# Optimization experiments

Measured on AMD Instinct MI355X. Metric: run time of the kernel, lower is better.

## Reference

```python
import jax, jax.numpy as jnp
import numpy as np

FEATURES, NEURONS, THETA, TAU, H = 128, 512, 256, 1.0, 0.1
B, T = 64, 2048

def setup_inputs() -> dict:
    key = jax.random.key(0)
    ks = jax.random.split(key, 8)
    IN = FEATURES + NEURONS
    s = lambda n: 1.0 / np.sqrt(n)
    return {
        "I": jax.random.normal(ks[0], (B, T, FEATURES), dtype=jnp.float32),
        "W_ih": jax.random.uniform(ks[1], (THETA, IN), jnp.float32, -s(THETA), s(THETA)),
        "W_hh": jax.random.uniform(ks[2], (THETA, THETA), jnp.float32, -s(THETA), s(THETA)),
        "b_ih": jax.random.uniform(ks[3], (THETA,), jnp.float32, -s(THETA), s(THETA)),
        "b_hh": jax.random.uniform(ks[4], (THETA,), jnp.float32, -s(THETA), s(THETA)),
        "W_out": jax.random.uniform(ks[5], (NEURONS, THETA), jnp.float32, -s(THETA), s(THETA)),
        "b_out": jax.random.uniform(ks[6], (NEURONS,), jnp.float32, -s(THETA), s(THETA)),
        "A": jax.random.normal(ks[7], (NEURONS,), dtype=jnp.float32),
    }

def reference(I, W_ih, W_hh, b_ih, b_hh, W_out, b_out, A):
    batch = I.shape[0]
    x0 = jnp.zeros((batch, NEURONS), I.dtype)
    s0 = jnp.zeros((batch, THETA), I.dtype)

    def step(carry, I_t):
        x, s = carry
        cat = jnp.concatenate([x, I_t], axis=-1)            # [B, neurons+features]
        s_new = jnp.tanh(cat @ W_ih.T + b_ih + s @ W_hh.T + b_hh)  # single-step tanh RNN
        f = jax.nn.relu(s_new @ W_out.T + b_out)            # [B, neurons]
        # implicit-Euler ODE update
        x_next = (x + H * (f * A)) / (1.0 + H * (1.0 / TAU + f))
        return (x_next, s_new), x_next

    _, xs = jax.lax.scan(step, (x0, s0), jnp.swapaxes(I, 0, 1))  # [T, B, neurons]
    return jnp.swapaxes(xs, 0, 1)  # [B, T, neurons]
```

## Files before the change

kernel.cpp:

```cpp
#include <hip/hip_runtime.h>
#include <hip/hip_fp16.h>

#define TT 2048
typedef unsigned int uint32;
typedef unsigned long long uint64;
typedef unsigned short ushort;

typedef _Float16 half2v __attribute__((ext_vector_type(2)));

#if defined(__has_builtin)
#  if __has_builtin(__builtin_amdgcn_fdot2)
#    define HAVE_DOT2 1
#  endif
#endif
#ifndef HAVE_DOT2
#  define HAVE_DOT2 0
#endif

#define WREG_N (2 * 176 * 512)
#define EXA_N  (2 * 64 * 2 * 256)

__device__ __forceinline__ float dot2(uint32 a, uint32 w, float c)
{
#if HAVE_DOT2
    return __builtin_amdgcn_fdot2(__builtin_bit_cast(half2v, a),
                                  __builtin_bit_cast(half2v, w), c, false);
#else
    half2v av = __builtin_bit_cast(half2v, a);
    half2v wv = __builtin_bit_cast(half2v, w);
    c = fmaf((float)av.x, (float)wv.x, c);
    return fmaf((float)av.y, (float)wv.y, c);
#endif
}

__device__ __forceinline__ uint32 pkh(float a, float b)
{
    __half ha = __float2half(a), hb = __float2half(b);
    ushort ua = *reinterpret_cast<ushort*>(&ha);
    ushort ub = *reinterpret_cast<ushort*>(&hb);
    return (uint32)ua | ((uint32)ub << 16);
}

__device__ __forceinline__ float getSlice(const float* __restrict__ W_ih,
                                          const float* __restrict__ W_hh,
                                          int g, int j, int k)
{
    if (k < 256) return W_ih[j * 640 + 256 * g + k];
    if (k < 384) return W_hh[j * 256 + 128 * g + (k - 256)];
    return W_ih[j * 640 + 512 + 64 * g + (k - 384)];
}

__global__ void prep_kernel(const float* __restrict__ W_ih,
                            const float* __restrict__ W_hh,
                            const float* __restrict__ W_out,
                            uint32* __restrict__ WREGH,
                            uint64* __restrict__ exS)
{
    int idx = blockIdx.x * blockDim.x + threadIdx.x;
    if (idx < WREG_N) {
        int tid  = idx & 511;
        int q    = idx >> 9;
        int g    = q / 176;
        int slot = q % 176;
        float lo, hi;
        if (slot < 112) {
            int j = tid >> 1, h = tid & 1;
            int k0 = 2 * (112 * h + slot);
            lo = getSlice(W_ih, W_hh, g, j, k0);
            hi = getSlice(W_ih, W_hh, g, j, k0 + 1);
        } else {
            int s  = slot - 112;
            int ii = s >> 2, m = s & 3;
            int nloc = tid >> 1, hh = tid & 1;
            int n  = 256 * g + nloc;
            int k0 = 128 * hh + 8 * ii + 2 * m;
            lo = W_out[n * 256 + k0];
            hi = W_out[n * 256 + k0 + 1];
        }
        WREGH[idx] = pkh(lo, hi);
    } else if (idx < WREG_N + EXA_N) {
        exS[idx - WREG_N] = 0ULL;
    }
}

__device__ __forceinline__ void bar_lds()
{
    asm volatile("s_waitcnt lgkmcnt(0)" ::: "memory");
    __builtin_amdgcn_s_barrier();
    asm volatile("" ::: "memory");
}

__global__ __launch_bounds__(512, 2)
void scan_kernel(const float* __restrict__ I,
                 const float* __restrict__ b_ih, const float* __restrict__ b_hh,
                 const float* __restrict__ b_out, const float* __restrict__ A,
                 const uint32* __restrict__ WREGH,
                 uint64* exS,
                 float* __restrict__ out)
{
    __shared__ uint4 apk4[2][56];
    __shared__ uint4 s4pk[32];
    __shared__ float xf32[256];

    const int tid = threadIdx.x;
    const int bid = blockIdx.x;
    const int b   = bid & 63;
    const int g   = bid >> 6;

    uint32 wA[112], wB[64];
    const uint32* wsrc = WREGH + (size_t)g * (176 * 512) + tid;
    #pragma unroll
    for (int i = 0; i < 112; ++i) { wA[i] = wsrc[(size_t)i * 512]; asm("" : "+v"(wA[i])); }
    #pragma unroll
    for (int i = 0; i < 64;  ++i) { wB[i] = wsrc[(size_t)(112 + i) * 512]; asm("" : "+v"(wB[i])); }

    const int h    = tid & 1;
    const int jA   = tid >> 1;
    const int hh   = tid & 1;
    const int nloc = tid >> 1;

    const float bs   = ((tid & 1) == 0) ? (b_ih[jA] + b_hh[jA]) : 0.f;
    const float bo_r = ((tid & 1) == 0) ? b_out[256 * g + nloc] : 0.f;
    const float Av_r = ((tid & 1) == 0) ? A[256 * g + nloc] : 0.f;

    const size_t iBase   = (size_t)b * TT * 128 + 64 * g;
    const size_t outBase = (size_t)b * TT * 512 + 256 * g;

    {
        uint32* a0p = (uint32*)&apk4[0][0];
        if (tid < 192) a0p[tid] = 0u;
        else if (tid < 224) {
            int m = tid - 192;
            a0p[tid] = pkh(I[iBase + 2 * m], I[iBase + 2 * m + 1]);
        }
        if (tid < 256) xf32[tid] = 0.f;
    }
    __syncthreads();

    for (int t = 0; t < TT; ++t) {
        const int par = t & 1;
        const uint4* rdp = apk4[par];
        uint32*      wrp = (uint32*)apk4[par ^ 1];

        float2 iv2 = make_float2(0.f, 0.f);
        if (tid < 32) {
            int tl = (t + 1 < TT) ? (t + 1) : t;
            iv2 = *(const float2*)(I + iBase + (size_t)tl * 128 + 2 * tid);
        }

        float a0 = 0.f, a1 = 0.f;
        #pragma unroll
        for (int i = 0; i < 28; ++i) {
            uint4 av = rdp[28 * h + i];
            a0 = dot2(av.x, wA[4 * i + 0], a0);
            a1 = dot2(av.y, wA[4 * i + 1], a1);
            a0 = dot2(av.z, wA[4 * i + 2], a0);
            a1 = dot2(av.w, wA[4 * i + 3], a1);
        }
        float acc = a0 + a1;
        acc += __shfl_xor(acc, 1);

        const uint32 tgt = (uint32)(t + 1);
        uint64* ex = exS + (size_t)(par * 64 + b) * (2 * 256);

        float sn = 0.f;
        if ((tid & 1) == 0) {
            uint64 u = ((uint64)tgt << 32) | (uint64)__float_as_uint(acc);
            __hip_atomic_store(ex + g * 256 + jA, u,
                               __ATOMIC_RELAXED, __HIP_MEMORY_SCOPE_AGENT);

            const uint64* pp = ex + (1 - g) * 256 + jA;
            uint64 up;
            do {
                up = __hip_atomic_load(pp, __ATOMIC_RELAXED, __HIP_MEMORY_SCOPE_AGENT);
            } while ((uint32)(up >> 32) != tgt);

            float pre = acc + bs + __uint_as_float((uint32)up);
            float e = __expf(2.f * pre);
            sn = 1.f - 2.f / (e + 1.f);
        }
        {
            float sno = __shfl_xor(sn, 2);
            if ((tid & 3) == 0) {
                int p = tid >> 2;
                uint32 sp = pkh(sn, sno);
                ((uint32*)s4pk)[p] = sp;
                int d = p - 64 * g;
                if (d >= 0 && d < 64) wrp[128 + d] = sp;
            }
        }
        bar_lds();

        float c0 = 0.f, c1 = 0.f;
        #pragma unroll
        for (int i = 0; i < 16; ++i) {
            uint4 sv = s4pk[16 * hh + i];
            c0 = dot2(sv.x, wB[4 * i + 0], c0);
            c1 = dot2(sv.y, wB[4 * i + 1], c1);
            c0 = dot2(sv.z, wB[4 * i + 2], c0);
            c1 = dot2(sv.w, wB[4 * i + 3], c1);
        }
        float f = c0 + c1;
        f += __shfl_xor(f, 1);

        float xn = 0.f;
        if ((tid & 1) == 0) {
            float ff = fmaxf(f + bo_r, 0.f);
            float xo = xf32[nloc];
            xn = (xo + 0.1f * ff * Av_r) / (1.1f + 0.1f * ff);
            xf32[nloc] = xn;
            out[outBase + (size_t)t * 512 + nloc] = xn;
        }
        {
            float xno = __shfl_xor(xn, 2);
            if ((tid & 3) == 0)
                wrp[tid >> 2] = pkh(xn, xno);
        }
        if (tid < 32) wrp[192 + tid] = pkh(iv2.x, iv2.y);
        bar_lds();
    }
}

extern "C" void kernel_launch(void* const* d_in, const int* in_sizes, int n_in,
                              void* d_out, int out_size, void* d_ws, size_t ws_size,
                              hipStream_t stream)
{
    const float* I     = (const float*)d_in[0];
    const float* W_ih  = (const float*)d_in[1];
    const float* W_hh  = (const float*)d_in[2];
    const float* b_ih  = (const float*)d_in[3];
    const float* b_hh  = (const float*)d_in[4];
    const float* W_out = (const float*)d_in[5];
    const float* b_out = (const float*)d_in[6];
    const float* A     = (const float*)d_in[7];

    uint32* WREGH = (uint32*)d_ws;
    uint64* exS   = (uint64*)((uint32*)d_ws + WREG_N);

    const int total = WREG_N + EXA_N;
    prep_kernel<<<(total + 1023) / 1024, 1024, 0, stream>>>(W_ih, W_hh, W_out,
                                                            WREGH, exS);
    scan_kernel<<<128, 512, 0, stream>>>(I, b_ih, b_hh, b_out, A,
                                         WREGH, exS, (float*)d_out);
}
```

Before: 4.453 ms.

## Pair co-located blocks on same XCD and exchange via sc0 L2-local path

```diff
diff --git a/kernel.cpp b/kernel.cpp
--- a/kernel.cpp
+++ b/kernel.cpp
@@ -18,7 +18,8 @@
 #endif
 
 #define WREG_N (2 * 176 * 512)
-#define EXA_N  (2 * 64 * 2 * 256)
+#define EX_N   (2 * 64 * 2 * 256)
+#define ZQ_N   (2 * EX_N + 256)
 
 __device__ __forceinline__ float dot2(uint32 a, uint32 w, float c)
 {
@@ -54,7 +55,7 @@
                             const float* __restrict__ W_hh,
                             const float* __restrict__ W_out,
                             uint32* __restrict__ WREGH,
-                            uint64* __restrict__ exS)
+                            uint64* __restrict__ zbase)
 {
     int idx = blockIdx.x * blockDim.x + threadIdx.x;
     if (idx < WREG_N) {
@@ -78,8 +79,8 @@
             hi = W_out[n * 256 + k0 + 1];
         }
         WREGH[idx] = pkh(lo, hi);
-    } else if (idx < WREG_N + EXA_N) {
-        exS[idx - WREG_N] = 0ULL;
+    } else if (idx < WREG_N + ZQ_N) {
+        zbase[idx - WREG_N] = 0ULL;
     }
 }
 
@@ -88,6 +89,29 @@
     asm volatile("s_waitcnt lgkmcnt(0)" ::: "memory");
     __builtin_amdgcn_s_barrier();
     asm volatile("" ::: "memory");
+}
+
+__device__ __forceinline__ void st64_sc0(uint64* p, uint64 v)
+{
+    asm volatile("global_store_dwordx2 %0, %1, off sc0" :: "v"(p), "v"(v) : "memory");
+}
+__device__ __forceinline__ uint64 ld64_sc0(const uint64* p)
+{
+    uint64 r;
+    asm volatile("global_load_dwordx2 %0, %1, off sc0\n\ts_waitcnt vmcnt(0)"
+                 : "=v"(r) : "v"(p) : "memory");
+    return r;
+}
+__device__ __forceinline__ void st32_sc0(uint32* p, uint32 v)
+{
+    asm volatile("global_store_dword %0, %1, off sc0" :: "v"(p), "v"(v) : "memory");
+}
+__device__ __forceinline__ uint32 ld32_sc0(const uint32* p)
+{
+    uint32 r;
+    asm volatile("global_load_dword %0, %1, off sc0\n\ts_waitcnt vmcnt(0)"
+                 : "=v"(r) : "v"(p) : "memory");
+    return r;
 }
 
 __global__ __launch_bounds__(512, 2)
@@ -95,17 +119,60 @@
                  const float* __restrict__ b_ih, const float* __restrict__ b_hh,
                  const float* __restrict__ b_out, const float* __restrict__ A,
                  const uint32* __restrict__ WREGH,
-                 uint64* exS,
+                 uint64* exS, uint64* exF, uint32* PS,
                  float* __restrict__ out)
 {
     __shared__ uint4 apk4[2][56];
     __shared__ uint4 s4pk[32];
     __shared__ float xf32[256];
+    __shared__ uint32 shInfo[2];
 
     const int tid = threadIdx.x;
-    const int bid = blockIdx.x;
-    const int b   = bid & 63;
-    const int g   = bid >> 6;
+
+    if (tid == 0) {
+        uint32 x;
+        asm volatile("s_getreg_b32 %0, hwreg(HW_REG_XCC_ID)" : "=s"(x));
+        x &= 7u;
+        uint32 rank = __hip_atomic_fetch_add(PS + x, 1u,
+                          __ATOMIC_RELAXED, __HIP_MEMORY_SCOPE_AGENT);
+        __hip_atomic_fetch_add(PS + 8, 1u, __ATOMIC_RELAXED, __HIP_MEMORY_SCOPE_AGENT);
+        while (__hip_atomic_load(PS + 8, __ATOMIC_RELAXED, __HIP_MEMORY_SCOPE_AGENT) < 128u)
+            __builtin_amdgcn_s_sleep(1);
+        uint32 cnt[8];
+        #pragma unroll
+        for (int i = 0; i < 8; ++i)
+            cnt[i] = __hip_atomic_load(PS + i, __ATOMIC_RELAXED, __HIP_MEMORY_SCOPE_AGENT);
+        uint32 totp = 0, cumB = 0, sB = 0;
+        #pragma unroll
+        for (int i = 0; i < 8; ++i) {
+            if ((uint32)i < x) { cumB += cnt[i] >> 1; sB += cnt[i] & 1; }
+            totp += cnt[i] >> 1;
+        }
+        uint32 e, g;
+        if (rank < 2u * (cnt[x] >> 1)) { e = cumB + (rank >> 1); g = rank & 1u; }
+        else                           { e = totp + (sB >> 1);   g = sB & 1u; }
+        uint32* pb = PS + 16  + 2 * e;
+        uint32* vt = PS + 160 + 2 * e;
+        const uint32 TOK = 0x5EEDF00Du;
+        st32_sc0(pb + g, TOK);
+        uint32 seen = 0;
+        for (int it = 0; it < 4096 && !seen; ++it)
+            seen = (ld32_sc0(pb + (1u - g)) == TOK) ? 1u : 0u;
+        __hip_atomic_store(vt + g, seen ? 2u : 1u,
+                           __ATOMIC_RELAXED, __HIP_MEMORY_SCOPE_AGENT);
+        uint32 v0, v1;
+        do {
+            v0 = __hip_atomic_load(vt + 0, __ATOMIC_RELAXED, __HIP_MEMORY_SCOPE_AGENT);
+            v1 = __hip_atomic_load(vt + 1, __ATOMIC_RELAXED, __HIP_MEMORY_SCOPE_AGENT);
+        } while (v0 == 0u || v1 == 0u);
+        shInfo[0] = e | (g << 16);
+        shInfo[1] = (v0 == 2u && v1 == 2u) ? 1u : 0u;
+    }
+    __syncthreads();
+    const int  e        = shInfo[0] & 0xffff;
+    const int  g        = shInfo[0] >> 16;
+    const bool fastpair = (shInfo[1] != 0);
+    bool fastok = fastpair;
 
     uint32 wA[112], wB[64];
     const uint32* wsrc = WREGH + (size_t)g * (176 * 512) + tid;
@@ -123,8 +190,8 @@
     const float bo_r = ((tid & 1) == 0) ? b_out[256 * g + nloc] : 0.f;
     const float Av_r = ((tid & 1) == 0) ? A[256 * g + nloc] : 0.f;
 
-    const size_t iBase   = (size_t)b * TT * 128 + 64 * g;
-    const size_t outBase = (size_t)b * TT * 512 + 256 * g;
+    const size_t iBase   = (size_t)e * TT * 128 + 64 * g;
+    const size_t outBase = (size_t)e * TT * 512 + 256 * g;
 
     {
         uint32* a0p = (uint32*)&apk4[0][0];
@@ -160,33 +227,43 @@
         float acc = a0 + a1;
         acc += __shfl_xor(acc, 1);
 
-        const uint32 tgt = (uint32)(t + 1);
-        uint64* ex = exS + (size_t)(par * 64 + b) * (2 * 256);
+        const uint32 tgt   = (uint32)(t + 1);
+        const size_t exoff = (size_t)(par * 64 + e) * (2 * 256);
 
         float sn = 0.f;
         if ((tid & 1) == 0) {
             uint64 u = ((uint64)tgt << 32) | (uint64)__float_as_uint(acc);
-            __hip_atomic_store(ex + g * 256 + jA, u,
+            if (fastpair) st64_sc0(exF + exoff + g * 256 + jA, u);
+            __hip_atomic_store(exS + exoff + g * 256 + jA, u,
                                __ATOMIC_RELAXED, __HIP_MEMORY_SCOPE_AGENT);
 
-            const uint64* pp = ex + (1 - g) * 256 + jA;
-            uint64 up;
-            do {
-                up = __hip_atomic_load(pp, __ATOMIC_RELAXED, __HIP_MEMORY_SCOPE_AGENT);
-            } while ((uint32)(up >> 32) != tgt);
+            const uint64* fp = exF + exoff + (1 - g) * 256 + jA;
+            const uint64* sp = exS + exoff + (1 - g) * 256 + jA;
+            uint64 up = 0; bool got = false;
+            if (fastok) {
+                for (int it = 0; it < 1024 && !got; ++it) {
+                    up = ld64_sc0(fp);
+                    got = ((uint32)(up >> 32) == tgt);
+                }
+                if (!got) fastok = false;
+            }
+            while (!got) {
+                up = __hip_atomic_load(sp, __ATOMIC_RELAXED, __HIP_MEMORY_SCOPE_AGENT);
+                got = ((uint32)(up >> 32) == tgt);
+            }
 
             float pre = acc + bs + __uint_as_float((uint32)up);
-            float e = __expf(2.f * pre);
-            sn = 1.f - 2.f / (e + 1.f);
+            float ex2 = __expf(2.f * pre);
+            sn = 1.f - 2.f / (ex2 + 1.f);
         }
         {
             float sno = __shfl_xor(sn, 2);
             if ((tid & 3) == 0) {
                 int p = tid >> 2;
-                uint32 sp = pkh(sn, sno);
-                ((uint32*)s4pk)[p] = sp;
+                uint32 sp2 = pkh(sn, sno);
+                ((uint32*)s4pk)[p] = sp2;
                 int d = p - 64 * g;
-                if (d >= 0 && d < 64) wrp[128 + d] = sp;
+                if (d >= 0 && d < 64) wrp[128 + d] = sp2;
             }
         }
         bar_lds();
@@ -235,11 +312,14 @@
     const float* A     = (const float*)d_in[7];
 
     uint32* WREGH = (uint32*)d_ws;
-    uint64* exS   = (uint64*)((uint32*)d_ws + WREG_N);
-
-    const int total = WREG_N + EXA_N;
+    uint64* zbase = (uint64*)((uint32*)d_ws + WREG_N);
+    uint64* exS   = zbase;
+    uint64* exF   = zbase + EX_N;
+    uint32* PS    = (uint32*)(zbase + 2 * EX_N);
+
+    const int total = WREG_N + ZQ_N;
     prep_kernel<<<(total + 1023) / 1024, 1024, 0, stream>>>(W_ih, W_hh, W_out,
-                                                            WREGH, exS);
+                                                            WREGH, zbase);
     scan_kernel<<<128, 512, 0, stream>>>(I, b_ih, b_hh, b_out, A,
-                                         WREGH, exS, (float*)d_out);
-}
+                                         WREGH, exS, exF, PS, (float*)d_out);
+}
```

Result: slower. 4.876 ms (+9.5%).
